# Performance work log

Measured on AMD Instinct MI355X. Metric: run time of the kernel, lower is better.

## Reference

```python
import jax, jax.numpy as jnp
import numpy as np

LN_EPS = 1e-5

def _layernorm(x, gamma, beta):
    mu = jnp.mean(x, axis=-1, keepdims=True)
    var = jnp.mean(jnp.square(x - mu), axis=-1, keepdims=True)
    return (x - mu) * jax.lax.rsqrt(var + LN_EPS) * gamma + beta

def setup_inputs() -> dict:
    key = jax.random.key(0)
    ks = jax.random.split(key, 10)
    d_model, outdim = 1024, 512
    n_support, n_queries = 8192, 8192
    s = 1.0 / np.sqrt(d_model)
    return {
        "support_set": jax.random.normal(ks[0], (n_support, d_model), jnp.float32),
        "queries": jax.random.normal(ks[1], (n_queries, d_model), jnp.float32),
        "Wq": jax.random.uniform(ks[2], (outdim, d_model), jnp.float32, -s, s),
        "bq": jax.random.uniform(ks[3], (outdim,), jnp.float32, -s, s),
        "Wk": jax.random.uniform(ks[4], (outdim, d_model), jnp.float32, -s, s),
        "bk": jax.random.uniform(ks[5], (outdim,), jnp.float32, -s, s),
        "Wv": jax.random.uniform(ks[6], (outdim, d_model), jnp.float32, -s, s),
        "bv": jax.random.uniform(ks[7], (outdim,), jnp.float32, -s, s),
        "ln_gamma": jnp.ones((outdim,), jnp.float32),
        "ln_beta": jnp.zeros((outdim,), jnp.float32),
    }

def reference(support_set, queries, Wq, bq, Wk, bk, Wv, bv, ln_gamma, ln_beta):
    outdim = Wq.shape[0]
    # V projections
    support_vs = support_set @ Wv.T + bv            # [Ns, O]
    q_prototype = queries @ Wv.T + bv               # [Nq, O]
    # QK projections, shared LayerNorm (norm_k applied to both)
    support_ks = _layernorm(support_set @ Wk.T + bk, ln_gamma, ln_beta)  # [Ns, O]
    queries_qs = _layernorm(queries @ Wq.T + bq, ln_gamma, ln_beta)     # [Nq, O]
    # scaled scores + softmax over support axis (dim=1)
    scores = (queries_qs @ support_ks.T) / jnp.sqrt(jnp.float32(outdim))  # [Nq, Ns]
    affinity = jax.nn.softmax(scores, axis=1)
    class_prototype = affinity @ support_vs         # [Nq, O]
    return (q_prototype, class_prototype)
```

## Files before the change

### kernel.cpp

```cpp
#include <hip/hip_runtime.h>
#include <hip/hip_bf16.h>

typedef __attribute__((ext_vector_type(8))) short bf16x8;
typedef __attribute__((ext_vector_type(4))) float f32x4;
typedef __attribute__((ext_vector_type(4))) short short4_t;
typedef __attribute__((ext_vector_type(4))) float float4_t;

#define MFMA16(a, b, c) __builtin_amdgcn_mfma_f32_16x16x32_bf16((a), (b), (c), 0, 0, 0)

__device__ __forceinline__ unsigned short f2bf(float f) {
    unsigned u = __builtin_bit_cast(unsigned, f);
    u += 0x7fffu + ((u >> 16) & 1u);
    return (unsigned short)(u >> 16);
}

__device__ __forceinline__ short4_t pack4(float4_t v) {
    short4_t r;
    r[0] = (short)f2bf(v[0]);
    r[1] = (short)f2bf(v[1]);
    r[2] = (short)f2bf(v[2]);
    r[3] = (short)f2bf(v[3]);
    return r;
}

__device__ __forceinline__ void gload_lds16(const void* g, void* l) {
    __builtin_amdgcn_global_load_lds(
        (const __attribute__((address_space(1))) unsigned int*)g,
        (__attribute__((address_space(3))) unsigned int*)l, 16, 0, 0);
}

__global__ __launch_bounds__(512, 2) void proj_v_kernel(
    const float* __restrict__ support, const float* __restrict__ queries,
    const float* __restrict__ Wv, const float* __restrict__ bv,
    float* __restrict__ q_proto, unsigned short* __restrict__ VsT)
{
    const int mode = blockIdx.x >> 7;
    const int rem = blockIdx.x & 127;
    const int rowbase = (rem >> 1) * 128;
    const int colbase = (rem & 1) * 256;
    const float* in = mode ? support : queries;

    const int t = threadIdx.x;
    const int w = t >> 6, l = t & 63, lg = l >> 4, ll = l & 15;
    const int wr = w & 1, wc = w >> 1;

    __shared__ unsigned short Alds[2][128][36];
    __shared__ unsigned short Blds[2][256][36];

    f32x4 acc[4][4];
    #pragma unroll
    for (int i = 0; i < 4; ++i)
        #pragma unroll
        for (int j = 0; j < 4; ++j) acc[i][j] = (f32x4){0.f, 0.f, 0.f, 0.f};

    const int srow = t >> 3, skc = (t & 7) * 4;
    const float* aptr = in + (size_t)(rowbase + srow) * 1024 + skc;
    const float* bptr = Wv + (size_t)(colbase + srow) * 1024 + skc;

    float4_t aReg[2], bReg[4];
    #pragma unroll
    for (int c = 0; c < 2; ++c) aReg[c] = *(const float4_t*)(aptr + (size_t)c * 64 * 1024);
    #pragma unroll
    for (int c = 0; c < 4; ++c) bReg[c] = *(const float4_t*)(bptr + (size_t)c * 64 * 1024);

    for (int kt = 0; kt < 32; ++kt) {
        const int cur = kt & 1;
        #pragma unroll
        for (int c = 0; c < 2; ++c)
            *(short4_t*)&Alds[cur][srow + c * 64][skc] = pack4(aReg[c]);
        #pragma unroll
        for (int c = 0; c < 4; ++c)
            *(short4_t*)&Blds[cur][srow + c * 64][skc] = pack4(bReg[c]);
        __syncthreads();
        if (kt < 31) {
            const int kb = (kt + 1) * 32;
            #pragma unroll
            for (int c = 0; c < 2; ++c) aReg[c] = *(const float4_t*)(aptr + (size_t)c * 64 * 1024 + kb);
            #pragma unroll
            for (int c = 0; c < 4; ++c) bReg[c] = *(const float4_t*)(bptr + (size_t)c * 64 * 1024 + kb);
        }
        bf16x8 af[4], bfr[4];
        #pragma unroll
        for (int mf = 0; mf < 4; ++mf) af[mf] = *(const bf16x8*)&Alds[cur][wr * 64 + mf * 16 + ll][lg * 8];
        #pragma unroll
        for (int nf = 0; nf < 4; ++nf) bfr[nf] = *(const bf16x8*)&Blds[cur][wc * 64 + nf * 16 + ll][lg * 8];
        #pragma unroll
        for (int mf = 0; mf < 4; ++mf)
            #pragma unroll
            for (int nf = 0; nf < 4; ++nf)
                acc[mf][nf] = MFMA16(af[mf], bfr[nf], acc[mf][nf]);
        __syncthreads();
    }

    float bvv[4];
    #pragma unroll
    for (int nf = 0; nf < 4; ++nf) bvv[nf] = bv[colbase + wc * 64 + nf * 16 + ll];

    if (mode == 0) {
        #pragma unroll
        for (int mf = 0; mf < 4; ++mf)
            #pragma unroll
            for (int r = 0; r < 4; ++r) {
                const size_t row = rowbase + wr * 64 + mf * 16 + lg * 4 + r;
                #pragma unroll
                for (int nf = 0; nf < 4; ++nf)
                    q_proto[row * 512 + colbase + wc * 64 + nf * 16 + ll] = acc[mf][nf][r] + bvv[nf];
            }
    } else {
        #pragma unroll
        for (int mf = 0; mf < 4; ++mf)
            #pragma unroll
            for (int nf = 0; nf < 4; ++nf) {
                float4_t pv = {acc[mf][nf][0] + bvv[nf], acc[mf][nf][1] + bvv[nf],
                               acc[mf][nf][2] + bvv[nf], acc[mf][nf][3] + bvv[nf]};
                const size_t col = colbase + wc * 64 + nf * 16 + ll;
                *(short4_t*)&VsT[col * 8192 + rowbase + wr * 64 + mf * 16 + lg * 4] = pack4(pv);
            }
    }
}

__global__ __launch_bounds__(512, 2) void proj_ln_kernel(
    const float* __restrict__ support, const float* __restrict__ queries,
    const float* __restrict__ Wk, const float* __restrict__ bk,
    const float* __restrict__ Wq, const float* __restrict__ bq,
    const float* __restrict__ gamma, const float* __restrict__ beta,
    unsigned short* __restrict__ Ks, unsigned short* __restrict__ Qs)
{
    const int mode = blockIdx.x >> 7;
    const int rowbase = (blockIdx.x & 127) * 64;
    const float* in = mode ? queries : support;
    const float* W = mode ? Wq : Wk;
    const float* bias = mode ? bq : bk;
    unsigned short* dst = mode ? Qs : Ks;

    const int t = threadIdx.x;
    const int w = t >> 6, l = t & 63, lg = l >> 4, ll = l & 15;
    const int wr = w & 1, wc = w >> 1;

    __shared__ unsigned short Alds[2][64][36];
    __shared__ unsigned short Blds[2][512][36];
    __shared__ float red[4][64][2];
    __shared__ float stats[64][2];

    f32x4 acc[2][8];
    #pragma unroll
    for (int i = 0; i < 2; ++i)
        #pragma unroll
        for (int j = 0; j < 8; ++j) acc[i][j] = (f32x4){0.f, 0.f, 0.f, 0.f};

    const int srow = t >> 3, skc = (t & 7) * 4;
    const float* aptr = in + (size_t)(rowbase + srow) * 1024 + skc;
    const float* bptr = W + (size_t)srow * 1024 + skc;

    float4_t aReg, bReg[8];
    aReg = *(const float4_t*)aptr;
    #pragma unroll
    for (int c = 0; c < 8; ++c) bReg[c] = *(const float4_t*)(bptr + (size_t)c * 64 * 1024);

    for (int kt = 0; kt < 32; ++kt) {
        const int cur = kt & 1;
        *(short4_t*)&Alds[cur][srow][skc] = pack4(aReg);
        #pragma unroll
        for (int c = 0; c < 8; ++c)
            *(short4_t*)&Blds[cur][srow + c * 64][skc] = pack4(bReg[c]);
        __syncthreads();
        if (kt < 31) {
            const int kb = (kt + 1) * 32;
            aReg = *(const float4_t*)(aptr + kb);
            #pragma unroll
            for (int c = 0; c < 8; ++c) bReg[c] = *(const float4_t*)(bptr + (size_t)c * 64 * 1024 + kb);
        }
        bf16x8 af[2], bfr[8];
        #pragma unroll
        for (int mf = 0; mf < 2; ++mf) af[mf] = *(const bf16x8*)&Alds[cur][wr * 32 + mf * 16 + ll][lg * 8];
        #pragma unroll
        for (int nf = 0; nf < 8; ++nf) bfr[nf] = *(const bf16x8*)&Blds[cur][wc * 128 + nf * 16 + ll][lg * 8];
        #pragma unroll
        for (int mf = 0; mf < 2; ++mf)
            #pragma unroll
            for (int nf = 0; nf < 8; ++nf)
                acc[mf][nf] = MFMA16(af[mf], bfr[nf], acc[mf][nf]);
        __syncthreads();
    }

    float bvv[8];
    #pragma unroll
    for (int nf = 0; nf < 8; ++nf) bvv[nf] = bias[wc * 128 + nf * 16 + ll];

    float v[2][8][4];
    #pragma unroll
    for (int mf = 0; mf < 2; ++mf)
        #pragma unroll
        for (int nf = 0; nf < 8; ++nf)
            #pragma unroll
            for (int r = 0; r < 4; ++r)
                v[mf][nf][r] = acc[mf][nf][r] + bvv[nf];

    #pragma unroll
    for (int mf = 0; mf < 2; ++mf)
        #pragma unroll
        for (int r = 0; r < 4; ++r) {
            float s = 0.f, q = 0.f;
            #pragma unroll
            for (int nf = 0; nf < 8; ++nf) { s += v[mf][nf][r]; q += v[mf][nf][r] * v[mf][nf][r]; }
            #pragma unroll
            for (int d = 1; d < 16; d <<= 1) { s += __shfl_xor(s, d); q += __shfl_xor(q, d); }
            if (ll == 0) {
                red[wc][wr * 32 + mf * 16 + lg * 4 + r][0] = s;
                red[wc][wr * 32 + mf * 16 + lg * 4 + r][1] = q;
            }
        }
    __syncthreads();
    if (t < 64) {
        float S = 0.f, Q = 0.f;
        #pragma unroll
        for (int w2 = 0; w2 < 4; ++w2) { S += red[w2][t][0]; Q += red[w2][t][1]; }
        const float mu = S * (1.f / 512.f);
        const float var = Q * (1.f / 512.f) - mu * mu;
        stats[t][0] = mu;
        stats[t][1] = rsqrtf(var + 1e-5f);
    }
    __syncthreads();
    float gv[8], bev[8];
    #pragma unroll
    for (int nf = 0; nf < 8; ++nf) {
        gv[nf] = gamma[wc * 128 + nf * 16 + ll];
        bev[nf] = beta[wc * 128 + nf * 16 + ll];
    }
    #pragma unroll
    for (int mf = 0; mf < 2; ++mf)
        #pragma unroll
        for (int r = 0; r < 4; ++r) {
            const int row = wr * 32 + mf * 16 + lg * 4 + r;
            const float mu = stats[row][0], rs = stats[row][1];
            #pragma unroll
            for (int nf = 0; nf < 8; ++nf) {
                const float o = (v[mf][nf][r] - mu) * rs * gv[nf] + bev[nf];
                dst[(size_t)(rowbase + row) * 512 + wc * 128 + nf * 16 + ll] = f2bf(o);
            }
        }
}

__global__ __launch_bounds__(512, 2) void attn_kernel(
    const unsigned short* __restrict__ Qs, const unsigned short* __restrict__ Ks,
    const unsigned short* __restrict__ VsT,
    float* __restrict__ Opart, float* __restrict__ lpart)
{
    const int bid = blockIdx.x;
    const int sp = (bid & 7) >> 2;
    const int qb = (bid >> 3) * 4 + (bid & 3);
    const int qbase = qb * 64;
    const int kv0 = sp * 4096;
    const int t = threadIdx.x;
    const int w = t >> 6, l = t & 63, lg = l >> 4, ll = l & 15;
    const int wq = w & 3, wk = w >> 2;

    __shared__ unsigned short Klds[2][64][512];
    __shared__ unsigned short Plds[2][64][64];
    __shared__ float lsum[2][64];

    bf16x8 qf[16];
    {
        const unsigned short* qrow = Qs + (size_t)(qbase + wq * 16 + ll) * 512 + lg * 8;
        #pragma unroll
        for (int ks = 0; ks < 16; ++ks)
            qf[ks] = *(const bf16x8*)(qrow + ks * 32);
    }

    f32x4 oacc[4][4];
    #pragma unroll
    for (int i = 0; i < 4; ++i)
        #pragma unroll
        for (int j = 0; j < 4; ++j) oacc[i][j] = (f32x4){0.f, 0.f, 0.f, 0.f};
    float lrun[4] = {0.f, 0.f, 0.f, 0.f};
    const float scale = 0.044194173824159216f;

    #pragma unroll
    for (int rr = 0; rr < 8; ++rr) {
        const int r = w * 8 + rr;
        gload_lds16(Ks + (size_t)(kv0 + r) * 512 + ((l ^ (r & 7)) << 3),
                    &Klds[0][r][0]);
    }
    __syncthreads();

    for (int it = 0; it < 64; ++it) {
        const int cur = it & 1;
        const int kvb = kv0 + it * 64;

        if (it < 63) {
            const int kvn = kvb + 64;
            #pragma unroll
            for (int rr = 0; rr < 8; ++rr) {
                const int r = w * 8 + rr;
                gload_lds16(Ks + (size_t)(kvn + r) * 512 + ((l ^ (r & 7)) << 3),
                            &Klds[cur ^ 1][r][0]);
            }
        }

        f32x4 sacc[2];
        sacc[0] = (f32x4){0.f, 0.f, 0.f, 0.f};
        sacc[1] = (f32x4){0.f, 0.f, 0.f, 0.f};
        __builtin_amdgcn_s_setprio(1);
        #pragma unroll
        for (int ks = 0; ks < 16; ++ks) {
            const int u = ((ks * 4 + lg) ^ (ll & 7)) * 8;
            #pragma unroll
            for (int nf = 0; nf < 2; ++nf) {
                bf16x8 kf = *(const bf16x8*)&Klds[cur][wk * 32 + nf * 16 + ll][u];
                sacc[nf] = MFMA16(qf[ks], kf, sacc[nf]);
            }
        }
        __builtin_amdgcn_s_setprio(0);

        bf16x8 vf[2][4];
        #pragma unroll
        for (int ks2 = 0; ks2 < 2; ++ks2)
            #pragma unroll
            for (int nf = 0; nf < 4; ++nf)
                vf[ks2][nf] = *(const bf16x8*)(VsT + (size_t)(w * 64 + nf * 16 + ll) * 8192
                                               + kvb + ks2 * 32 + lg * 8);

        #pragma unroll
        for (int r = 0; r < 4; ++r) {
            const int row = wq * 16 + lg * 4 + r;
            const int swz = (row >> 1) & 7;
            float rsum = 0.f;
            #pragma unroll
            for (int nf = 0; nf < 2; ++nf) {
                const float p = __expf(sacc[nf][r] * scale);
                rsum += p;
                const int col = wk * 32 + nf * 16 + ll;
                const int unit = (col >> 3) ^ swz;
                Plds[cur][row][unit * 8 + (col & 7)] = f2bf(p);
            }
            #pragma unroll
            for (int d = 1; d < 16; d <<= 1) rsum += __shfl_xor(rsum, d);
            lrun[r] += rsum;
        }

        __syncthreads();

        __builtin_amdgcn_s_setprio(1);
        #pragma unroll
        for (int ks2 = 0; ks2 < 2; ++ks2) {
            #pragma unroll
            for (int mf = 0; mf < 4; ++mf) {
                const int row = mf * 16 + ll;
                const int unit = (ks2 * 4 + lg) ^ ((row >> 1) & 7);
                bf16x8 pf = *(const bf16x8*)&Plds[cur][row][unit * 8];
                #pragma unroll
                for (int nf = 0; nf < 4; ++nf)
                    oacc[mf][nf] = MFMA16(pf, vf[ks2][nf], oacc[mf][nf]);
            }
        }
        __builtin_amdgcn_s_setprio(0);
    }

    const size_t obase = (size_t)sp * 8192 + qbase;
    #pragma unroll
    for (int mf = 0; mf < 4; ++mf)
        #pragma unroll
        for (int r = 0; r < 4; ++r) {
            const size_t row = obase + mf * 16 + lg * 4 + r;
            #pragma unroll
            for (int nf = 0; nf < 4; ++nf)
                Opart[row * 512 + w * 64 + nf * 16 + ll] = oacc[mf][nf][r];
        }
    if (ll == 0) {
        #pragma unroll
        for (int r = 0; r < 4; ++r)
            lsum[wk][wq * 16 + lg * 4 + r] = lrun[r];
    }
    __syncthreads();
    if (t < 64)
        lpart[(size_t)sp * 8192 + qbase + t] = lsum[0][t] + lsum[1][t];
}

__global__ __launch_bounds__(256) void merge_kernel(
    const float* __restrict__ Opart, const float* __restrict__ lpart,
    float* __restrict__ out2)
{
    const int idx = blockIdx.x * 256 + threadIdx.x;
    const int q = idx >> 7;
    const int c = (idx & 127) * 4;
    float4_t a = {0.f, 0.f, 0.f, 0.f};
    float ls = 0.f;
    #pragma unroll
    for (int s = 0; s < 2; ++s) {
        float4_t vv = *(const float4_t*)(Opart + ((size_t)s * 8192 + q) * 512 + c);
        a += vv;
        ls += lpart[s * 8192 + q];
    }
    const float inv = 1.f / ls;
    *(float4_t*)(out2 + (size_t)q * 512 + c) = a * inv;
}

extern "C" void kernel_launch(void* const* d_in, const int* in_sizes, int n_in,
                              void* d_out, int out_size, void* d_ws, size_t ws_size,
                              hipStream_t stream)
{
    const float* support = (const float*)d_in[0];
    const float* queries = (const float*)d_in[1];
    const float* Wq = (const float*)d_in[2];
    const float* bq = (const float*)d_in[3];
    const float* Wk = (const float*)d_in[4];
    const float* bk = (const float*)d_in[5];
    const float* Wv = (const float*)d_in[6];
    const float* bv = (const float*)d_in[7];
    const float* gamma = (const float*)d_in[8];
    const float* beta = (const float*)d_in[9];

    float* out = (float*)d_out;
    float* q_proto = out;
    float* out2 = out + (size_t)8192 * 512;

    char* ws = (char*)d_ws;
    unsigned short* Qs  = (unsigned short*)(ws);
    unsigned short* Ks  = (unsigned short*)(ws + ((size_t)8 << 20));
    unsigned short* VsT = (unsigned short*)(ws + ((size_t)16 << 20));
    float* Opart = (float*)(ws + ((size_t)24 << 20));
    float* lpart = (float*)(ws + ((size_t)56 << 20));

    proj_v_kernel<<<256, 512, 0, stream>>>(support, queries, Wv, bv, q_proto, VsT);
    proj_ln_kernel<<<256, 512, 0, stream>>>(support, queries, Wk, bk, Wq, bq,
                                            gamma, beta, Ks, Qs);
    attn_kernel<<<256, 512, 0, stream>>>(Qs, Ks, VsT, Opart, lpart);
    merge_kernel<<<4096, 256, 0, stream>>>(Opart, lpart, out2);
}
```

Baseline: 295.6 us.

## Precast inputs to bf16 and stream projection tiles via async global-to-LDS loads

Adds a cast kernel that converts support, queries and the three weight matrices to bf16 once. The projection kernels then load bf16 tiles directly into swizzled LDS with global_load_lds, using a 64-wide K step and double buffering in place of register-staged fp32 loads with per-tile packing. The LN projection wave layout changes to 8 column-wise waves, and the attention kernel regroups waves so each K fragment feeds two query fragments. This costs an extra pass over the inputs and workspace for the bf16 copies; Opart reuses the same workspace region as the bf16 support and query copies, which is safe only because those copies are dead before the attention kernel runs.

```diff
diff --git a/kernel.cpp b/kernel.cpp
--- a/kernel.cpp
+++ b/kernel.cpp
@@ -4,6 +4,7 @@
 typedef __attribute__((ext_vector_type(8))) short bf16x8;
 typedef __attribute__((ext_vector_type(4))) float f32x4;
 typedef __attribute__((ext_vector_type(4))) short short4_t;
+typedef __attribute__((ext_vector_type(8))) short short8_t;
 typedef __attribute__((ext_vector_type(4))) float float4_t;
 
 #define MFMA16(a, b, c) __builtin_amdgcn_mfma_f32_16x16x32_bf16((a), (b), (c), 0, 0, 0)
@@ -29,23 +30,48 @@
         (__attribute__((address_space(3))) unsigned int*)l, 16, 0, 0);
 }
 
+__global__ __launch_bounds__(256) void cast_kernel(
+    const float* __restrict__ support, const float* __restrict__ queries,
+    const float* __restrict__ Wq, const float* __restrict__ Wk,
+    const float* __restrict__ Wv,
+    unsigned short* __restrict__ sb, unsigned short* __restrict__ qb,
+    unsigned short* __restrict__ wqb, unsigned short* __restrict__ wkb,
+    unsigned short* __restrict__ wvb)
+{
+    const size_t e = ((size_t)blockIdx.x * 256 + threadIdx.x) * 8;
+    const float* src; unsigned short* dst; size_t off;
+    if (e < 8388608)       { src = support; dst = sb;  off = e; }
+    else if (e < 16777216) { src = queries; dst = qb;  off = e - 8388608; }
+    else if (e < 17301504) { src = Wq;      dst = wqb; off = e - 16777216; }
+    else if (e < 17825792) { src = Wk;      dst = wkb; off = e - 17301504; }
+    else                   { src = Wv;      dst = wvb; off = e - 17825792; }
+    float4_t a = *(const float4_t*)(src + off);
+    float4_t b = *(const float4_t*)(src + off + 4);
+    short4_t lo = pack4(a), hi = pack4(b);
+    short8_t o;
+    o[0] = lo[0]; o[1] = lo[1]; o[2] = lo[2]; o[3] = lo[3];
+    o[4] = hi[0]; o[5] = hi[1]; o[6] = hi[2]; o[7] = hi[3];
+    *(short8_t*)(dst + off) = o;
+}
+
 __global__ __launch_bounds__(512, 2) void proj_v_kernel(
-    const float* __restrict__ support, const float* __restrict__ queries,
-    const float* __restrict__ Wv, const float* __restrict__ bv,
+    const unsigned short* __restrict__ sb, const unsigned short* __restrict__ qb,
+    const unsigned short* __restrict__ wvb, const float* __restrict__ bv,
     float* __restrict__ q_proto, unsigned short* __restrict__ VsT)
 {
     const int mode = blockIdx.x >> 7;
     const int rem = blockIdx.x & 127;
     const int rowbase = (rem >> 1) * 128;
     const int colbase = (rem & 1) * 256;
-    const float* in = mode ? support : queries;
+    const unsigned short* A = mode ? sb : qb;
 
     const int t = threadIdx.x;
     const int w = t >> 6, l = t & 63, lg = l >> 4, ll = l & 15;
     const int wr = w & 1, wc = w >> 1;
-
-    __shared__ unsigned short Alds[2][128][36];
-    __shared__ unsigned short Blds[2][256][36];
+    const int sr = l >> 3, su = l & 7;
+
+    __shared__ unsigned short Alds[2][128][64];
+    __shared__ unsigned short Blds[2][256][64];
 
     f32x4 acc[4][4];
     #pragma unroll
@@ -53,44 +79,50 @@
         #pragma unroll
         for (int j = 0; j < 4; ++j) acc[i][j] = (f32x4){0.f, 0.f, 0.f, 0.f};
 
-    const int srow = t >> 3, skc = (t & 7) * 4;
-    const float* aptr = in + (size_t)(rowbase + srow) * 1024 + skc;
-    const float* bptr = Wv + (size_t)(colbase + srow) * 1024 + skc;
-
-    float4_t aReg[2], bReg[4];
-    #pragma unroll
-    for (int c = 0; c < 2; ++c) aReg[c] = *(const float4_t*)(aptr + (size_t)c * 64 * 1024);
-    #pragma unroll
-    for (int c = 0; c < 4; ++c) bReg[c] = *(const float4_t*)(bptr + (size_t)c * 64 * 1024);
-
-    for (int kt = 0; kt < 32; ++kt) {
+    #define PV_STAGE(buf, kt)                                                   \
+        {                                                                       \
+            const int kc = (kt) * 64;                                           \
+            _Pragma("unroll")                                                   \
+            for (int g = 0; g < 2; ++g) {                                       \
+                const int r0 = w * 16 + g * 8, row = r0 + sr;                   \
+                gload_lds16(A + (size_t)(rowbase + row) * 1024 + kc             \
+                                + ((su ^ (row & 7)) << 3),                      \
+                            &Alds[buf][r0][0]);                                 \
+            }                                                                   \
+            _Pragma("unroll")                                                   \
+            for (int g = 0; g < 4; ++g) {                                       \
+                const int r0 = w * 32 + g * 8, row = r0 + sr;                   \
+                gload_lds16(wvb + (size_t)(colbase + row) * 1024 + kc           \
+                                + ((su ^ (row & 7)) << 3),                      \
+                            &Blds[buf][r0][0]);                                 \
+            }                                                                   \
+        }
+
+    PV_STAGE(0, 0)
+    __syncthreads();
+
+    for (int kt = 0; kt < 16; ++kt) {
         const int cur = kt & 1;
-        #pragma unroll
-        for (int c = 0; c < 2; ++c)
-            *(short4_t*)&Alds[cur][srow + c * 64][skc] = pack4(aReg[c]);
-        #pragma unroll
-        for (int c = 0; c < 4; ++c)
-            *(short4_t*)&Blds[cur][srow + c * 64][skc] = pack4(bReg[c]);
+        if (kt < 15) PV_STAGE(cur ^ 1, kt + 1)
+        #pragma unroll
+        for (int ks = 0; ks < 2; ++ks) {
+            const int u = ((ks * 4 + lg) ^ (ll & 7)) * 8;
+            bf16x8 af[4], bfr[4];
+            #pragma unroll
+            for (int mf = 0; mf < 4; ++mf)
+                af[mf] = *(const bf16x8*)&Alds[cur][wr * 64 + mf * 16 + ll][u];
+            #pragma unroll
+            for (int nf = 0; nf < 4; ++nf)
+                bfr[nf] = *(const bf16x8*)&Blds[cur][wc * 64 + nf * 16 + ll][u];
+            #pragma unroll
+            for (int mf = 0; mf < 4; ++mf)
+                #pragma unroll
+                for (int nf = 0; nf < 4; ++nf)
+                    acc[mf][nf] = MFMA16(af[mf], bfr[nf], acc[mf][nf]);
+        }
         __syncthreads();
-        if (kt < 31) {
-            const int kb = (kt + 1) * 32;
-            #pragma unroll
-            for (int c = 0; c < 2; ++c) aReg[c] = *(const float4_t*)(aptr + (size_t)c * 64 * 1024 + kb);
-            #pragma unroll
-            for (int c = 0; c < 4; ++c) bReg[c] = *(const float4_t*)(bptr + (size_t)c * 64 * 1024 + kb);
-        }
-        bf16x8 af[4], bfr[4];
-        #pragma unroll
-        for (int mf = 0; mf < 4; ++mf) af[mf] = *(const bf16x8*)&Alds[cur][wr * 64 + mf * 16 + ll][lg * 8];
-        #pragma unroll
-        for (int nf = 0; nf < 4; ++nf) bfr[nf] = *(const bf16x8*)&Blds[cur][wc * 64 + nf * 16 + ll][lg * 8];
-        #pragma unroll
-        for (int mf = 0; mf < 4; ++mf)
-            #pragma unroll
-            for (int nf = 0; nf < 4; ++nf)
-                acc[mf][nf] = MFMA16(af[mf], bfr[nf], acc[mf][nf]);
-        __syncthreads();
-    }
+    }
+    #undef PV_STAGE
 
     float bvv[4];
     #pragma unroll
@@ -120,123 +152,132 @@
 }
 
 __global__ __launch_bounds__(512, 2) void proj_ln_kernel(
-    const float* __restrict__ support, const float* __restrict__ queries,
-    const float* __restrict__ Wk, const float* __restrict__ bk,
-    const float* __restrict__ Wq, const float* __restrict__ bq,
+    const unsigned short* __restrict__ sb, const unsigned short* __restrict__ qb,
+    const unsigned short* __restrict__ wkb, const float* __restrict__ bk,
+    const unsigned short* __restrict__ wqb, const float* __restrict__ bq,
     const float* __restrict__ gamma, const float* __restrict__ beta,
     unsigned short* __restrict__ Ks, unsigned short* __restrict__ Qs)
 {
     const int mode = blockIdx.x >> 7;
     const int rowbase = (blockIdx.x & 127) * 64;
-    const float* in = mode ? queries : support;
-    const float* W = mode ? Wq : Wk;
+    const unsigned short* A = mode ? qb : sb;
+    const unsigned short* W = mode ? wqb : wkb;
     const float* bias = mode ? bq : bk;
     unsigned short* dst = mode ? Qs : Ks;
 
     const int t = threadIdx.x;
     const int w = t >> 6, l = t & 63, lg = l >> 4, ll = l & 15;
-    const int wr = w & 1, wc = w >> 1;
-
-    __shared__ unsigned short Alds[2][64][36];
-    __shared__ unsigned short Blds[2][512][36];
-    __shared__ float red[4][64][2];
+    const int sr = l >> 3, su = l & 7;
+
+    __shared__ unsigned short Alds[2][64][64];
+    __shared__ unsigned short Blds[2][512][64];
+    __shared__ float red[8][64][2];
     __shared__ float stats[64][2];
 
-    f32x4 acc[2][8];
-    #pragma unroll
-    for (int i = 0; i < 2; ++i)
-        #pragma unroll
-        for (int j = 0; j < 8; ++j) acc[i][j] = (f32x4){0.f, 0.f, 0.f, 0.f};
-
-    const int srow = t >> 3, skc = (t & 7) * 4;
-    const float* aptr = in + (size_t)(rowbase + srow) * 1024 + skc;
-    const float* bptr = W + (size_t)srow * 1024 + skc;
-
-    float4_t aReg, bReg[8];
-    aReg = *(const float4_t*)aptr;
-    #pragma unroll
-    for (int c = 0; c < 8; ++c) bReg[c] = *(const float4_t*)(bptr + (size_t)c * 64 * 1024);
-
-    for (int kt = 0; kt < 32; ++kt) {
+    f32x4 acc[4][4];
+    #pragma unroll
+    for (int i = 0; i < 4; ++i)
+        #pragma unroll
+        for (int j = 0; j < 4; ++j) acc[i][j] = (f32x4){0.f, 0.f, 0.f, 0.f};
+
+    #define LN_STAGE(buf, kt)                                                   \
+        {                                                                       \
+            const int kc = (kt) * 64;                                           \
+            {                                                                   \
+                const int r0 = w * 8, row = r0 + sr;                            \
+                gload_lds16(A + (size_t)(rowbase + row) * 1024 + kc             \
+                                + ((su ^ (row & 7)) << 3),                      \
+                            &Alds[buf][r0][0]);                                 \
+            }                                                                   \
+            _Pragma("unroll")                                                   \
+            for (int g = 0; g < 8; ++g) {                                       \
+                const int r0 = w * 64 + g * 8, row = r0 + sr;                   \
+                gload_lds16(W + (size_t)row * 1024 + kc                         \
+                                + ((su ^ (row & 7)) << 3),                      \
+                            &Blds[buf][r0][0]);                                 \
+            }                                                                   \
+        }
+
+    LN_STAGE(0, 0)
+    __syncthreads();
+
+    for (int kt = 0; kt < 16; ++kt) {
         const int cur = kt & 1;
-        *(short4_t*)&Alds[cur][srow][skc] = pack4(aReg);
-        #pragma unroll
-        for (int c = 0; c < 8; ++c)
-            *(short4_t*)&Blds[cur][srow + c * 64][skc] = pack4(bReg[c]);
+        if (kt < 15) LN_STAGE(cur ^ 1, kt + 1)
+        #pragma unroll
+        for (int ks = 0; ks < 2; ++ks) {
+            const int u = ((ks * 4 + lg) ^ (ll & 7)) * 8;
+            bf16x8 af[4], bfr[4];
+            #pragma unroll
+            for (int mf = 0; mf < 4; ++mf)
+                af[mf] = *(const bf16x8*)&Alds[cur][mf * 16 + ll][u];
+            #pragma unroll
+            for (int nf = 0; nf < 4; ++nf)
+                bfr[nf] = *(const bf16x8*)&Blds[cur][w * 64 + nf * 16 + ll][u];
+            #pragma unroll
+            for (int mf = 0; mf < 4; ++mf)
+                #pragma unroll
+                for (int nf = 0; nf < 4; ++nf)
+                    acc[mf][nf] = MFMA16(af[mf], bfr[nf], acc[mf][nf]);
+        }
         __syncthreads();
-        if (kt < 31) {
-            const int kb = (kt + 1) * 32;
-            aReg = *(const float4_t*)(aptr + kb);
-            #pragma unroll
-            for (int c = 0; c < 8; ++c) bReg[c] = *(const float4_t*)(bptr + (size_t)c * 64 * 1024 + kb);
-        }
-        bf16x8 af[2], bfr[8];
-        #pragma unroll
-        for (int mf = 0; mf < 2; ++mf) af[mf] = *(const bf16x8*)&Alds[cur][wr * 32 + mf * 16 + ll][lg * 8];
-        #pragma unroll
-        for (int nf = 0; nf < 8; ++nf) bfr[nf] = *(const bf16x8*)&Blds[cur][wc * 128 + nf * 16 + ll][lg * 8];
-        #pragma unroll
-        for (int mf = 0; mf < 2; ++mf)
-            #pragma unroll
-            for (int nf = 0; nf < 8; ++nf)
-                acc[mf][nf] = MFMA16(af[mf], bfr[nf], acc[mf][nf]);
-        __syncthreads();
-    }
-
-    float bvv[8];
-    #pragma unroll
-    for (int nf = 0; nf < 8; ++nf) bvv[nf] = bias[wc * 128 + nf * 16 + ll];
-
-    float v[2][8][4];
-    #pragma unroll
-    for (int mf = 0; mf < 2; ++mf)
-        #pragma unroll
-        for (int nf = 0; nf < 8; ++nf)
+    }
+    #undef LN_STAGE
+
+    float bvv[4];
+    #pragma unroll
+    for (int nf = 0; nf < 4; ++nf) bvv[nf] = bias[w * 64 + nf * 16 + ll];
+
+    float v[4][4][4];
+    #pragma unroll
+    for (int mf = 0; mf < 4; ++mf)
+        #pragma unroll
+        for (int nf = 0; nf < 4; ++nf)
             #pragma unroll
             for (int r = 0; r < 4; ++r)
                 v[mf][nf][r] = acc[mf][nf][r] + bvv[nf];
 
     #pragma unroll
-    for (int mf = 0; mf < 2; ++mf)
+    for (int mf = 0; mf < 4; ++mf)
         #pragma unroll
         for (int r = 0; r < 4; ++r) {
             float s = 0.f, q = 0.f;
             #pragma unroll
-            for (int nf = 0; nf < 8; ++nf) { s += v[mf][nf][r]; q += v[mf][nf][r] * v[mf][nf][r]; }
+            for (int nf = 0; nf < 4; ++nf) { s += v[mf][nf][r]; q += v[mf][nf][r] * v[mf][nf][r]; }
             #pragma unroll
             for (int d = 1; d < 16; d <<= 1) { s += __shfl_xor(s, d); q += __shfl_xor(q, d); }
             if (ll == 0) {
-                red[wc][wr * 32 + mf * 16 + lg * 4 + r][0] = s;
-                red[wc][wr * 32 + mf * 16 + lg * 4 + r][1] = q;
+                red[w][mf * 16 + lg * 4 + r][0] = s;
+                red[w][mf * 16 + lg * 4 + r][1] = q;
             }
         }
     __syncthreads();
     if (t < 64) {
         float S = 0.f, Q = 0.f;
         #pragma unroll
-        for (int w2 = 0; w2 < 4; ++w2) { S += red[w2][t][0]; Q += red[w2][t][1]; }
+        for (int w2 = 0; w2 < 8; ++w2) { S += red[w2][t][0]; Q += red[w2][t][1]; }
         const float mu = S * (1.f / 512.f);
         const float var = Q * (1.f / 512.f) - mu * mu;
         stats[t][0] = mu;
         stats[t][1] = rsqrtf(var + 1e-5f);
     }
     __syncthreads();
-    float gv[8], bev[8];
-    #pragma unroll
-    for (int nf = 0; nf < 8; ++nf) {
-        gv[nf] = gamma[wc * 128 + nf * 16 + ll];
-        bev[nf] = beta[wc * 128 + nf * 16 + ll];
-    }
-    #pragma unroll
-    for (int mf = 0; mf < 2; ++mf)
+    float gv[4], bev[4];
+    #pragma unroll
+    for (int nf = 0; nf < 4; ++nf) {
+        gv[nf] = gamma[w * 64 + nf * 16 + ll];
+        bev[nf] = beta[w * 64 + nf * 16 + ll];
+    }
+    #pragma unroll
+    for (int mf = 0; mf < 4; ++mf)
         #pragma unroll
         for (int r = 0; r < 4; ++r) {
-            const int row = wr * 32 + mf * 16 + lg * 4 + r;
+            const int row = mf * 16 + lg * 4 + r;
             const float mu = stats[row][0], rs = stats[row][1];
             #pragma unroll
-            for (int nf = 0; nf < 8; ++nf) {
+            for (int nf = 0; nf < 4; ++nf) {
                 const float o = (v[mf][nf][r] - mu) * rs * gv[nf] + bev[nf];
-                dst[(size_t)(rowbase + row) * 512 + wc * 128 + nf * 16 + ll] = f2bf(o);
+                dst[(size_t)(rowbase + row) * 512 + w * 64 + nf * 16 + ll] = f2bf(o);
             }
         }
 }
@@ -253,18 +294,19 @@
     const int kv0 = sp * 4096;
     const int t = threadIdx.x;
     const int w = t >> 6, l = t & 63, lg = l >> 4, ll = l & 15;
-    const int wq = w & 3, wk = w >> 2;
+    const int wq2 = w & 1, wk4 = w >> 1;
 
     __shared__ unsigned short Klds[2][64][512];
     __shared__ unsigned short Plds[2][64][64];
-    __shared__ float lsum[2][64];
-
-    bf16x8 qf[16];
-    {
-        const unsigned short* qrow = Qs + (size_t)(qbase + wq * 16 + ll) * 512 + lg * 8;
+    __shared__ float lsum[4][64];
+
+    bf16x8 qf[2][16];
+    #pragma unroll
+    for (int mf = 0; mf < 2; ++mf) {
+        const unsigned short* qrow = Qs + (size_t)(qbase + wq2 * 32 + mf * 16 + ll) * 512 + lg * 8;
         #pragma unroll
         for (int ks = 0; ks < 16; ++ks)
-            qf[ks] = *(const bf16x8*)(qrow + ks * 32);
+            qf[mf][ks] = *(const bf16x8*)(qrow + ks * 32);
     }
 
     f32x4 oacc[4][4];
@@ -272,7 +314,11 @@
     for (int i = 0; i < 4; ++i)
         #pragma unroll
         for (int j = 0; j < 4; ++j) oacc[i][j] = (f32x4){0.f, 0.f, 0.f, 0.f};
-    float lrun[4] = {0.f, 0.f, 0.f, 0.f};
+    float lrun[2][4];
+    #pragma unroll
+    for (int i = 0; i < 2; ++i)
+        #pragma unroll
+        for (int j = 0; j < 4; ++j) lrun[i][j] = 0.f;
     const float scale = 0.044194173824159216f;
 
     #pragma unroll
@@ -304,45 +350,38 @@
         #pragma unroll
         for (int ks = 0; ks < 16; ++ks) {
             const int u = ((ks * 4 + lg) ^ (ll & 7)) * 8;
-            #pragma unroll
-            for (int nf = 0; nf < 2; ++nf) {
-                bf16x8 kf = *(const bf16x8*)&Klds[cur][wk * 32 + nf * 16 + ll][u];
-                sacc[nf] = MFMA16(qf[ks], kf, sacc[nf]);
-            }
+            bf16x8 kf = *(const bf16x8*)&Klds[cur][wk4 * 16 + ll][u];
+            sacc[0] = MFMA16(qf[0][ks], kf, sacc[0]);
+            sacc[1] = MFMA16(qf[1][ks], kf, sacc[1]);
         }
         __builtin_amdgcn_s_setprio(0);
 
-        bf16x8 vf[2][4];
-        #pragma unroll
-        for (int ks2 = 0; ks2 < 2; ++ks2)
-            #pragma unroll
-            for (int nf = 0; nf < 4; ++nf)
-                vf[ks2][nf] = *(const bf16x8*)(VsT + (size_t)(w * 64 + nf * 16 + ll) * 8192
-                                               + kvb + ks2 * 32 + lg * 8);
-
-        #pragma unroll
-        for (int r = 0; r < 4; ++r) {
-            const int row = wq * 16 + lg * 4 + r;
-            const int swz = (row >> 1) & 7;
-            float rsum = 0.f;
-            #pragma unroll
-            for (int nf = 0; nf < 2; ++nf) {
-                const float p = __expf(sacc[nf][r] * scale);
-                rsum += p;
-                const int col = wk * 32 + nf * 16 + ll;
+        #pragma unroll
+        for (int mf = 0; mf < 2; ++mf)
+            #pragma unroll
+            for (int r = 0; r < 4; ++r) {
+                const int row = wq2 * 32 + mf * 16 + lg * 4 + r;
+                const int swz = (row >> 1) & 7;
+                const float p = __expf(sacc[mf][r] * scale);
+                const int col = wk4 * 16 + ll;
                 const int unit = (col >> 3) ^ swz;
                 Plds[cur][row][unit * 8 + (col & 7)] = f2bf(p);
-            }
-            #pragma unroll
-            for (int d = 1; d < 16; d <<= 1) rsum += __shfl_xor(rsum, d);
-            lrun[r] += rsum;
-        }
+                float rsum = p;
+                #pragma unroll
+                for (int d = 1; d < 16; d <<= 1) rsum += __shfl_xor(rsum, d);
+                lrun[mf][r] += rsum;
+            }
 
         __syncthreads();
 
         __builtin_amdgcn_s_setprio(1);
         #pragma unroll
         for (int ks2 = 0; ks2 < 2; ++ks2) {
+            bf16x8 vf[4];
+            #pragma unroll
+            for (int nf = 0; nf < 4; ++nf)
+                vf[nf] = *(const bf16x8*)(VsT + (size_t)(w * 64 + nf * 16 + ll) * 8192
+                                          + kvb + ks2 * 32 + lg * 8);
             #pragma unroll
             for (int mf = 0; mf < 4; ++mf) {
                 const int row = mf * 16 + ll;
@@ -350,7 +389,7 @@
                 bf16x8 pf = *(const bf16x8*)&Plds[cur][row][unit * 8];
                 #pragma unroll
                 for (int nf = 0; nf < 4; ++nf)
-                    oacc[mf][nf] = MFMA16(pf, vf[ks2][nf], oacc[mf][nf]);
+                    oacc[mf][nf] = MFMA16(pf, vf[nf], oacc[mf][nf]);
             }
         }
         __builtin_amdgcn_s_setprio(0);
@@ -368,12 +407,15 @@
         }
     if (ll == 0) {
         #pragma unroll
-        for (int r = 0; r < 4; ++r)
-            lsum[wk][wq * 16 + lg * 4 + r] = lrun[r];
+        for (int mf = 0; mf < 2; ++mf)
+            #pragma unroll
+            for (int r = 0; r < 4; ++r)
+                lsum[wk4][wq2 * 32 + mf * 16 + lg * 4 + r] = lrun[mf][r];
     }
     __syncthreads();
     if (t < 64)
-        lpart[(size_t)sp * 8192 + qbase + t] = lsum[0][t] + lsum[1][t];
+        lpart[(size_t)sp * 8192 + qbase + t] =
+            lsum[0][t] + lsum[1][t] + lsum[2][t] + lsum[3][t];
 }
 
 __global__ __launch_bounds__(256) void merge_kernel(
@@ -418,11 +460,18 @@
     unsigned short* Qs  = (unsigned short*)(ws);
     unsigned short* Ks  = (unsigned short*)(ws + ((size_t)8 << 20));
     unsigned short* VsT = (unsigned short*)(ws + ((size_t)16 << 20));
+    unsigned short* sb  = (unsigned short*)(ws + ((size_t)24 << 20));
+    unsigned short* qbuf= (unsigned short*)(ws + ((size_t)40 << 20));
+    unsigned short* wqb = (unsigned short*)(ws + ((size_t)56 << 20));
+    unsigned short* wkb = (unsigned short*)(ws + ((size_t)57 << 20));
+    unsigned short* wvb = (unsigned short*)(ws + ((size_t)58 << 20));
     float* Opart = (float*)(ws + ((size_t)24 << 20));
-    float* lpart = (float*)(ws + ((size_t)56 << 20));
-
-    proj_v_kernel<<<256, 512, 0, stream>>>(support, queries, Wv, bv, q_proto, VsT);
-    proj_ln_kernel<<<256, 512, 0, stream>>>(support, queries, Wk, bk, Wq, bq,
+    float* lpart = (float*)(ws + ((size_t)59 << 20));
+
+    cast_kernel<<<8960, 256, 0, stream>>>(support, queries, Wq, Wk, Wv,
+                                          sb, qbuf, wqb, wkb, wvb);
+    proj_v_kernel<<<256, 512, 0, stream>>>(sb, qbuf, wvb, bv, q_proto, VsT);
+    proj_ln_kernel<<<256, 512, 0, stream>>>(sb, qbuf, wkb, bk, wqb, bq,
                                             gamma, beta, Ks, Qs);
     attn_kernel<<<256, 512, 0, stream>>>(Qs, Ks, VsT, Opart, lpart);
     merge_kernel<<<4096, 256, 0, stream>>>(Opart, lpart, out2);
```

Result: slower. 401.0 us (+35.6%).
